# Kernel tuning notes

Hardware: AMD Instinct MI355X
Metric: run time of the kernel (lower is better)

## Reference

```python
import jax, jax.numpy as jnp
import numpy as np

H = 1024; NH = 16; HD = H // NH  # hidden, heads, head_dim

def setup_inputs() -> dict:
    key = jax.random.key(0)
    ks = jax.random.split(key, 9)
    s = 1.0 / np.sqrt(H)
    return {
        "hidden_states": jax.random.normal(ks[0], (2, 2048, H), jnp.float32),
        "Wq": jax.random.uniform(ks[1], (H, H), jnp.float32, -s, s),
        "bq": jnp.zeros((H,), jnp.float32),
        "Wk": jax.random.uniform(ks[2], (H, H), jnp.float32, -s, s),
        "bk": jnp.zeros((H,), jnp.float32),
        "Wv": jax.random.uniform(ks[3], (H, H), jnp.float32, -s, s),
        "bv": jnp.zeros((H,), jnp.float32),
        "Wo": jax.random.uniform(ks[4], (H, H), jnp.float32, -s, s),
        "bo": jnp.zeros((H,), jnp.float32),
    }

def reference(hidden_states, Wq, bq, Wk, bk, Wv, bv, Wo, bo):
    B, S, _ = hidden_states.shape
    def heads(x):  # [B,S,H] -> [B,NH,S,HD]
        return x.reshape(B, S, NH, HD).transpose(0, 2, 1, 3)
    q = heads(hidden_states @ Wq + bq)
    k = heads(hidden_states @ Wk + bk)
    v = heads(hidden_states @ Wv + bv)
    scores = jnp.einsum('bhqd,bhkd->bhqk', q, k) / jnp.sqrt(jnp.float32(HD))
    causal = jnp.where(jnp.tril(jnp.ones((S, S), bool)), 0.0, -jnp.inf)
    probs = jax.nn.softmax(scores + causal[None, None], axis=-1)
    ctx = jnp.einsum('bhqk,bhkd->bhqd', probs, v)
    ctx = ctx.transpose(0, 2, 1, 3).reshape(B, S, H)
    return ctx @ Wo + bo
```

## Files before the change

### kernel.cpp

```cpp
#include <hip/hip_runtime.h>
#include <hip/hip_bf16.h>

#define BB 2
#define SS 2048
#define HH 1024
#define NHH 16
#define HDD 64
#define MM (BB*SS)
#define QKV_N (3*HH)

typedef _Float16 f16x8 __attribute__((ext_vector_type(8)));
typedef _Float16 f16x4 __attribute__((ext_vector_type(4)));
typedef float f32x4 __attribute__((ext_vector_type(4)));

#define MFMA16(a,b,c)  __builtin_amdgcn_mfma_f32_16x16x32_f16((a),(b),(c),0,0,0)
#define MFMA16K16(a,b,c) __builtin_amdgcn_mfma_f32_16x16x16f16((a),(b),(c),0,0,0)

__device__ __forceinline__ void gl2lds16(const _Float16* g, _Float16* l) {
    __builtin_amdgcn_global_load_lds(
        (const __attribute__((address_space(1))) void*)g,
        (__attribute__((address_space(3))) void*)l, 16, 0, 0);
}

__device__ __forceinline__ float fexp2(float x) { return __builtin_amdgcn_exp2f(x); }

__global__ __launch_bounds__(256) void prep_kernel(
    const float* __restrict__ X,
    const float* __restrict__ W0, const float* __restrict__ W1,
    const float* __restrict__ W2, const float* __restrict__ W3,
    _Float16* __restrict__ Xh,
    _Float16* __restrict__ WqkvT, _Float16* __restrict__ WoT)
{
    __shared__ float t[64][65];
    int z = blockIdx.z;
    int tid = threadIdx.x;
    if (z == 4) {
        int base = (blockIdx.y * 16 + blockIdx.x) * 256 + tid;
        const float4* xin = (const float4*)X;
        f16x4* xout = (f16x4*)Xh;
#pragma unroll
        for (int i = 0; i < 16; ++i) {
            float4 v = xin[base + i * 65536];
            f16x4 hh = {(_Float16)v.x, (_Float16)v.y, (_Float16)v.z, (_Float16)v.w};
            xout[base + i * 65536] = hh;
        }
        return;
    }
    const float* src = (z == 0) ? W0 : (z == 1) ? W1 : (z == 2) ? W2 : W3;
    _Float16* dst = (z < 3) ? (WqkvT + (size_t)z * HH * HH) : WoT;
    int k0 = blockIdx.y * 64, n0 = blockIdx.x * 64;
#pragma unroll
    for (int p = 0; p < 4; ++p) {
        int row = p * 16 + (tid >> 4);
        int col4 = (tid & 15) * 4;
        float4 v = *(const float4*)&src[(size_t)(k0 + row) * HH + n0 + col4];
        t[row][col4 + 0] = v.x; t[row][col4 + 1] = v.y;
        t[row][col4 + 2] = v.z; t[row][col4 + 3] = v.w;
    }
    __syncthreads();
#pragma unroll
    for (int p = 0; p < 2; ++p) {
        int nc = p * 32 + (tid >> 3);
        int ch = tid & 7;
        f16x8 o;
#pragma unroll
        for (int j = 0; j < 8; ++j) o[j] = (_Float16)t[ch * 8 + j][nc];
        *(f16x8*)&dst[(size_t)(n0 + nc) * HH + k0 + ch * 8] = o;
    }
}

__global__ __launch_bounds__(256, 5) void gemm_qkv_kernel(
    const _Float16* __restrict__ A, const _Float16* __restrict__ Bt,
    const float* __restrict__ bias0, const float* __restrict__ bias1, const float* __restrict__ bias2,
    _Float16* __restrict__ Qh, _Float16* __restrict__ Kh, _Float16* __restrict__ Vt)
{
    const int K = HH;
    const int NT = K / 32;
    __shared__ _Float16 smem[16384];

    int row0 = blockIdx.y * 128, n0 = blockIdx.x * 128;
    int tid = threadIdx.x;
    int w = tid >> 6, l = tid & 63, m16 = l & 15, quad = l >> 4;
    int wm = w >> 1, wn = w & 1;

    int srow = w * 32 + (l >> 2);
    int sch = (l & 3) ^ ((l >> 2) & 3) ^ ((l >> 4) & 3);
    const _Float16* aptr = A + (size_t)(row0 + srow) * K + sch * 8;
    const _Float16* bptr = Bt + (size_t)(n0 + srow) * K + sch * 8;

    int gsw = (m16 & 3) ^ ((m16 >> 2) & 3);
    int acol = (quad ^ gsw) * 8;

    f32x4 zero4 = {0.f, 0.f, 0.f, 0.f};
    f32x4 acc[4][4];
#pragma unroll
    for (int i = 0; i < 4; ++i)
#pragma unroll
        for (int j = 0; j < 4; ++j) acc[i][j] = zero4;

    auto stage = [&](int t) {
        int s = (t & 1) * 4096;
        int k0 = t * 32;
        int ao = s + (w * 32) * 32;
        int bo = 8192 + s + (w * 32) * 32;
        gl2lds16(aptr + k0, smem + ao);
        gl2lds16(aptr + (size_t)16 * K + k0, smem + ao + 16 * 32);
        gl2lds16(bptr + k0, smem + bo);
        gl2lds16(bptr + (size_t)16 * K + k0, smem + bo + 16 * 32);
    };

    stage(0);
    for (int t = 0; t < NT; ++t) {
        asm volatile("s_barrier" ::: "memory");
        if (t + 1 < NT) {
            stage(t + 1);
            asm volatile("s_waitcnt vmcnt(4)" ::: "memory");
        } else {
            asm volatile("s_waitcnt vmcnt(0)" ::: "memory");
        }
        asm volatile("s_barrier" ::: "memory");

        const _Float16* Asr = smem + (t & 1) * 4096;
        const _Float16* Bsr = smem + 8192 + (t & 1) * 4096;
        f16x8 af[4], bf[4];
#pragma unroll
        for (int i = 0; i < 4; ++i)
            af[i] = *(const f16x8*)&Asr[(wm * 64 + i * 16 + m16) * 32 + acol];
#pragma unroll
        for (int j = 0; j < 4; ++j)
            bf[j] = *(const f16x8*)&Bsr[(wn * 64 + j * 16 + m16) * 32 + acol];
#pragma unroll
        for (int i = 0; i < 4; ++i)
#pragma unroll
            for (int j = 0; j < 4; ++j)
                acc[i][j] = MFMA16(af[i], bf[j], acc[i][j]);
    }

    int which = n0 >> 10;
    const float* bias = (which == 0) ? bias0 : (which == 1) ? bias1 : bias2;
    int b = row0 >> 11, s0 = row0 & 2047;

#pragma unroll
    for (int rh = 0; rh < 2; ++rh) {
        __syncthreads();
        if (wm == rh) {
#pragma unroll
            for (int j = 0; j < 4; ++j) {
                int n_local = wn * 64 + j * 16 + m16;
                float bi = bias[(n0 + n_local) & 1023];
#pragma unroll
                for (int i = 0; i < 4; ++i)
#pragma unroll
                    for (int r = 0; r < 4; ++r) {
                        int m_loc = i * 16 + quad * 4 + r;
                        float v = acc[i][j][r] + bi;
                        if (which == 0) v *= 0.18033688011112042f;
                        if (which == 2) smem[n_local * 68 + m_loc] = (_Float16)v;
                        else            smem[m_loc * 132 + n_local] = (_Float16)v;
                    }
            }
        }
        __syncthreads();
        int hs0 = s0 + rh * 64;
        if (which == 2) {
#pragma unroll
            for (int p = 0; p < 4; ++p) {
                int n_local = p * 32 + (tid >> 3);
                int schunk = tid & 7;
                f16x8 v = *(const f16x8*)&smem[n_local * 68 + schunk * 8];
                int nw = (n0 + n_local) & 1023;
                int hh = nw >> 6, d = nw & 63;
                *(f16x8*)&Vt[((size_t)(b * NHH + hh) * HDD + d) * SS + hs0 + schunk * 8] = v;
            }
        } else {
            _Float16* dst = (which == 0) ? Qh : Kh;
            int hh0 = (n0 & 1023) >> 6;
#pragma unroll
            for (int p = 0; p < 4; ++p) {
                int m_local = p * 16 + (tid >> 4);
                int seg = tid & 15;
                f16x8 v = *(const f16x8*)&smem[m_local * 132 + seg * 8];
                int hh = hh0 + (seg >> 3), d = (seg & 7) * 8;
                *(f16x8*)&dst[((size_t)(b * NHH + hh) * SS + hs0 + m_local) * HDD + d] = v;
            }
        }
    }
}

__global__ __launch_bounds__(256) void gemm_out_kernel(
    const _Float16* __restrict__ A, const _Float16* __restrict__ Bt,
    const float* __restrict__ bias0, float* __restrict__ Out)
{
    const int K = HH;
    const int NT = K / 32;
    __shared__ _Float16 smem[24576];

    int row0 = blockIdx.y * 128, n0 = blockIdx.x * 128;
    int tid = threadIdx.x;
    int w = tid >> 6, l = tid & 63, m16 = l & 15, quad = l >> 4;
    int wm = w >> 1, wn = w & 1;

    int srow = w * 32 + (l >> 2);
    int sch = (l & 3) ^ ((l >> 2) & 3) ^ ((l >> 4) & 3);
    const _Float16* aptr = A + (size_t)(row0 + srow) * K + sch * 8;
    const _Float16* bptr = Bt + (size_t)(n0 + srow) * K + sch * 8;

    int gsw = (m16 & 3) ^ ((m16 >> 2) & 3);
    int acol = (quad ^ gsw) * 8;

    f32x4 zero4 = {0.f, 0.f, 0.f, 0.f};
    f32x4 acc[4][4];
#pragma unroll
    for (int i = 0; i < 4; ++i)
#pragma unroll
        for (int j = 0; j < 4; ++j) acc[i][j] = zero4;

    auto stage = [&](int t, int s) {
        int k0 = t * 32;
        int ao = s * 4096 + (w * 32) * 32;
        int bo = 12288 + s * 4096 + (w * 32) * 32;
        gl2lds16(aptr + k0, smem + ao);
        gl2lds16(aptr + (size_t)16 * K + k0, smem + ao + 16 * 32);
        gl2lds16(bptr + k0, smem + bo);
        gl2lds16(bptr + (size_t)16 * K + k0, smem + bo + 16 * 32);
    };

    stage(0, 0);
    stage(1, 1);
    int cur = 0;
    for (int t = 0; t < NT; ++t) {
        if (t < NT - 1) asm volatile("s_waitcnt vmcnt(4)" ::: "memory");
        else            asm volatile("s_waitcnt vmcnt(0)" ::: "memory");
        asm volatile("s_barrier" ::: "memory");
        if (t + 2 < NT) {
            int nxt = cur + 2; if (nxt >= 3) nxt -= 3;
            stage(t + 2, nxt);
        }
        const _Float16* Asr = smem + cur * 4096;
        const _Float16* Bsr = smem + 12288 + cur * 4096;
        f16x8 af[4], bf[4];
#pragma unroll
        for (int i = 0; i < 4; ++i)
            af[i] = *(const f16x8*)&Asr[(wm * 64 + i * 16 + m16) * 32 + acol];
#pragma unroll
        for (int j = 0; j < 4; ++j)
            bf[j] = *(const f16x8*)&Bsr[(wn * 64 + j * 16 + m16) * 32 + acol];
#pragma unroll
        for (int i = 0; i < 4; ++i)
#pragma unroll
            for (int j = 0; j < 4; ++j)
                acc[i][j] = MFMA16(af[i], bf[j], acc[i][j]);
        cur = (cur == 2) ? 0 : cur + 1;
    }

#pragma unroll
    for (int j = 0; j < 4; ++j) {
        int n = n0 + wn * 64 + j * 16 + m16;
        float bi = bias0[n];
#pragma unroll
        for (int i = 0; i < 4; ++i)
#pragma unroll
            for (int r = 0; r < 4; ++r) {
                int mg = row0 + wm * 64 + i * 16 + quad * 4 + r;
                Out[(size_t)mg * HH + n] = acc[i][j][r] + bi;
            }
    }
}

__global__ __launch_bounds__(512, 4) void attn_kernel(
    const _Float16* __restrict__ Qh, const _Float16* __restrict__ Kh,
    const _Float16* __restrict__ Vt, _Float16* __restrict__ Ctx)
{
    __shared__ _Float16 KV[3 * 8192];

    int tid = threadIdx.x;
    int w = tid >> 6, l = tid & 63;
    int m16 = l & 15, quad = l >> 4;
    int b = blockIdx.z, h = blockIdx.y;
    int tA = blockIdx.x, tB = 31 - tA;
    int half = w >> 2, wq = w & 3;
    int myT = half ? tB : tA;

    const _Float16* Q = Qh + (size_t)(b * NHH + h) * SS * HDD;
    const _Float16* K = Kh + (size_t)(b * NHH + h) * SS * HDD;
    const _Float16* V = Vt + (size_t)(b * NHH + h) * HDD * SS;

    int q = myT * 64 + wq * 16 + m16;
    f16x8 aq0 = *(const f16x8*)(Q + (size_t)q * HDD + quad * 8);
    f16x8 aq1 = *(const f16x8*)(Q + (size_t)q * HDD + 32 + quad * 8);

    int srow = w * 8 + (l >> 3);
    int sch = (l & 7) ^ (l >> 3);
    const _Float16* kg = K + (size_t)srow * HDD + sch * 8;
    const _Float16* vg = V + (size_t)srow * SS + sch * 8;

    auto stage = [&](int t, int s) {
        int kt = t * 64;
        _Float16* kb = &KV[s * 8192];
        _Float16* vb = &KV[s * 8192 + 4096];
        gl2lds16(kg + (size_t)kt * HDD, kb + (w * 8) * 64);
        gl2lds16(vg + kt, vb + (w * 8) * 64);
    };

    int swz = m16 & 7;
    int cka = (quad ^ swz) * 8;
    int ckb = ((quad + 4) ^ swz) * 8;
    int vco[4];
#pragma unroll
    for (int s = 0; s < 4; ++s)
        vco[s] = (((s * 2 + (quad >> 1)) ^ swz) * 8) + (quad & 1) * 4;

    f32x4 zero4 = {0.f, 0.f, 0.f, 0.f};
    const f16x4 ones4 = {(_Float16)1.f, (_Float16)1.f, (_Float16)1.f, (_Float16)1.f};
    f32x4 o[4];
#pragma unroll
    for (int c = 0; c < 4; ++c) o[c] = zero4;
    f32x4 lacc = zero4;

    stage(0, 0);
    stage(1, 1);
    int cur = 0;
    for (int t = 0; t <= tB; ++t) {
        int kt = t * 64;
        if (t < tB) asm volatile("s_waitcnt vmcnt(2)" ::: "memory");
        else        asm volatile("s_waitcnt vmcnt(0)" ::: "memory");
        asm volatile("s_barrier" ::: "memory");
        if (t + 2 <= tB) {
            int nxt = cur + 2; if (nxt >= 3) nxt -= 3;
            stage(t + 2, nxt);
        }

        if (t <= myT) {
            const _Float16* kb = &KV[cur * 8192];
            const _Float16* vb = &KV[cur * 8192 + 4096];
            f16x8 bk[4][2];
#pragma unroll
            for (int s = 0; s < 4; ++s) {
                const _Float16* kr = kb + (s * 16 + m16) * 64;
                bk[s][0] = *(const f16x8*)(kr + cka);
                bk[s][1] = *(const f16x8*)(kr + ckb);
            }
            f16x4 av[4][4];
#pragma unroll
            for (int c = 0; c < 4; ++c) {
                const _Float16* vr = vb + (c * 16 + m16) * 64;
#pragma unroll
                for (int s = 0; s < 4; ++s)
                    av[c][s] = *(const f16x4*)(vr + vco[s]);
            }

            f32x4 st[4];
#pragma unroll
            for (int s = 0; s < 4; ++s) {
                st[s] = MFMA16(bk[s][0], aq0, zero4);
                st[s] = MFMA16(bk[s][1], aq1, st[s]);
            }
            f16x4 pt[4];
            if (t == myT) {
#pragma unroll
                for (int s = 0; s < 4; ++s)
#pragma unroll
                    for (int r = 0; r < 4; ++r) {
                        float p = fexp2(st[s][r]);
                        int key = kt + s * 16 + quad * 4 + r;
                        if (key > q) p = 0.f;
                        pt[s][r] = (_Float16)p;
                    }
            } else {
#pragma unroll
                for (int s = 0; s < 4; ++s)
#pragma unroll
                    for (int r = 0; r < 4; ++r)
                        pt[s][r] = (_Float16)fexp2(st[s][r]);
            }
#pragma unroll
            for (int s = 0; s < 4; ++s)
                lacc = MFMA16K16(ones4, pt[s], lacc);
#pragma unroll
            for (int c = 0; c < 4; ++c)
#pragma unroll
                for (int s = 0; s < 4; ++s)
                    o[c] = MFMA16K16(av[c][s], pt[s], o[c]);
        }

        cur = (cur == 2) ? 0 : cur + 1;
    }

    float inv = 1.0f / lacc[0];
    size_t rowoff = ((size_t)(b * SS) + q) * HH + h * HDD;
#pragma unroll
    for (int c = 0; c < 4; ++c) {
        f16x4 ov;
#pragma unroll
        for (int r = 0; r < 4; ++r) ov[r] = (_Float16)(o[c][r] * inv);
        *(f16x4*)&Ctx[rowoff + c * 16 + quad * 4] = ov;
    }
}

extern "C" void kernel_launch(void* const* d_in, const int* in_sizes, int n_in,
                              void* d_out, int out_size, void* d_ws, size_t ws_size,
                              hipStream_t stream) {
    const float* hs = (const float*)d_in[0];
    const float* Wq = (const float*)d_in[1];
    const float* bq = (const float*)d_in[2];
    const float* Wk = (const float*)d_in[3];
    const float* bk = (const float*)d_in[4];
    const float* Wv = (const float*)d_in[5];
    const float* bv = (const float*)d_in[6];
    const float* Wo = (const float*)d_in[7];
    const float* bo = (const float*)d_in[8];
    float* out = (float*)d_out;

    size_t off = 0;
    auto alloc = [&](size_t bytes) {
        void* p = (char*)d_ws + off;
        off += (bytes + 255) & ~(size_t)255;
        return p;
    };
    _Float16* Xh    = (_Float16*)alloc((size_t)MM * HH * 2);
    _Float16* WqkvT = (_Float16*)alloc((size_t)3 * HH * HH * 2);
    _Float16* WoT   = (_Float16*)alloc((size_t)HH * HH * 2);
    _Float16* Qh    = (_Float16*)alloc((size_t)BB * NHH * SS * HDD * 2);
    _Float16* Kh    = (_Float16*)alloc((size_t)BB * NHH * SS * HDD * 2);
    _Float16* Vt    = (_Float16*)alloc((size_t)BB * NHH * SS * HDD * 2);
    _Float16* Ctx   = (_Float16*)alloc((size_t)MM * HH * 2);

    prep_kernel<<<dim3(16, 16, 5), 256, 0, stream>>>(
        hs, Wq, Wk, Wv, Wo, Xh, WqkvT, WoT);
    gemm_qkv_kernel<<<dim3(QKV_N / 128, MM / 128), 256, 0, stream>>>(
        Xh, WqkvT, bq, bk, bv, Qh, Kh, Vt);
    attn_kernel<<<dim3(16, NHH, BB), 512, 0, stream>>>(Qh, Kh, Vt, Ctx);
    gemm_out_kernel<<<dim3(HH / 128, MM / 128), 256, 0, stream>>>(
        Ctx, WoT, bo, out);
}
```

Measured before the change: 181.3 us.

## Split-K output GEMM with atomics, reuse out-GEMM pipeline for QKV, pair attention tiles

The output projection GEMM is split along K into two halves, and the partial sums are accumulated into a zeroed output with atomicAdd. The zeroing is added as a new z-slice of the prep kernel. The QKV GEMM now uses the 3-stage pipelined body from the out GEMM, with a single full-tile epilogue. The attention kernel now has both wave groups process both query tiles over alternating key tiles from a shared double-buffered pair, then merges partial outputs through LDS. This aims to raise parallelism and balance work, at the cost of atomic traffic and extra LDS reductions.

```diff
diff --git a/kernel.cpp b/kernel.cpp
--- a/kernel.cpp
+++ b/kernel.cpp
@@ -29,7 +29,8 @@
     const float* __restrict__ W0, const float* __restrict__ W1,
     const float* __restrict__ W2, const float* __restrict__ W3,
     _Float16* __restrict__ Xh,
-    _Float16* __restrict__ WqkvT, _Float16* __restrict__ WoT)
+    _Float16* __restrict__ WqkvT, _Float16* __restrict__ WoT,
+    float* __restrict__ OutZ)
 {
     __shared__ float t[64][65];
     int z = blockIdx.z;
@@ -46,6 +47,14 @@
         }
         return;
     }
+    if (z == 5) {
+        int base = (blockIdx.y * 16 + blockIdx.x) * 256 + tid;
+        float4* o4 = (float4*)OutZ;
+        float4 zv = {0.f, 0.f, 0.f, 0.f};
+#pragma unroll
+        for (int i = 0; i < 16; ++i) o4[base + i * 65536] = zv;
+        return;
+    }
     const float* src = (z == 0) ? W0 : (z == 1) ? W1 : (z == 2) ? W2 : W3;
     _Float16* dst = (z < 3) ? (WqkvT + (size_t)z * HH * HH) : WoT;
     int k0 = blockIdx.y * 64, n0 = blockIdx.x * 64;
@@ -69,127 +78,10 @@
     }
 }
 
-__global__ __launch_bounds__(256, 5) void gemm_qkv_kernel(
+__global__ __launch_bounds__(256) void gemm_qkv_kernel(
     const _Float16* __restrict__ A, const _Float16* __restrict__ Bt,
     const float* __restrict__ bias0, const float* __restrict__ bias1, const float* __restrict__ bias2,
     _Float16* __restrict__ Qh, _Float16* __restrict__ Kh, _Float16* __restrict__ Vt)
-{
-    const int K = HH;
-    const int NT = K / 32;
-    __shared__ _Float16 smem[16384];
-
-    int row0 = blockIdx.y * 128, n0 = blockIdx.x * 128;
-    int tid = threadIdx.x;
-    int w = tid >> 6, l = tid & 63, m16 = l & 15, quad = l >> 4;
-    int wm = w >> 1, wn = w & 1;
-
-    int srow = w * 32 + (l >> 2);
-    int sch = (l & 3) ^ ((l >> 2) & 3) ^ ((l >> 4) & 3);
-    const _Float16* aptr = A + (size_t)(row0 + srow) * K + sch * 8;
-    const _Float16* bptr = Bt + (size_t)(n0 + srow) * K + sch * 8;
-
-    int gsw = (m16 & 3) ^ ((m16 >> 2) & 3);
-    int acol = (quad ^ gsw) * 8;
-
-    f32x4 zero4 = {0.f, 0.f, 0.f, 0.f};
-    f32x4 acc[4][4];
-#pragma unroll
-    for (int i = 0; i < 4; ++i)
-#pragma unroll
-        for (int j = 0; j < 4; ++j) acc[i][j] = zero4;
-
-    auto stage = [&](int t) {
-        int s = (t & 1) * 4096;
-        int k0 = t * 32;
-        int ao = s + (w * 32) * 32;
-        int bo = 8192 + s + (w * 32) * 32;
-        gl2lds16(aptr + k0, smem + ao);
-        gl2lds16(aptr + (size_t)16 * K + k0, smem + ao + 16 * 32);
-        gl2lds16(bptr + k0, smem + bo);
-        gl2lds16(bptr + (size_t)16 * K + k0, smem + bo + 16 * 32);
-    };
-
-    stage(0);
-    for (int t = 0; t < NT; ++t) {
-        asm volatile("s_barrier" ::: "memory");
-        if (t + 1 < NT) {
-            stage(t + 1);
-            asm volatile("s_waitcnt vmcnt(4)" ::: "memory");
-        } else {
-            asm volatile("s_waitcnt vmcnt(0)" ::: "memory");
-        }
-        asm volatile("s_barrier" ::: "memory");
-
-        const _Float16* Asr = smem + (t & 1) * 4096;
-        const _Float16* Bsr = smem + 8192 + (t & 1) * 4096;
-        f16x8 af[4], bf[4];
-#pragma unroll
-        for (int i = 0; i < 4; ++i)
-            af[i] = *(const f16x8*)&Asr[(wm * 64 + i * 16 + m16) * 32 + acol];
-#pragma unroll
-        for (int j = 0; j < 4; ++j)
-            bf[j] = *(const f16x8*)&Bsr[(wn * 64 + j * 16 + m16) * 32 + acol];
-#pragma unroll
-        for (int i = 0; i < 4; ++i)
-#pragma unroll
-            for (int j = 0; j < 4; ++j)
-                acc[i][j] = MFMA16(af[i], bf[j], acc[i][j]);
-    }
-
-    int which = n0 >> 10;
-    const float* bias = (which == 0) ? bias0 : (which == 1) ? bias1 : bias2;
-    int b = row0 >> 11, s0 = row0 & 2047;
-
-#pragma unroll
-    for (int rh = 0; rh < 2; ++rh) {
-        __syncthreads();
-        if (wm == rh) {
-#pragma unroll
-            for (int j = 0; j < 4; ++j) {
-                int n_local = wn * 64 + j * 16 + m16;
-                float bi = bias[(n0 + n_local) & 1023];
-#pragma unroll
-                for (int i = 0; i < 4; ++i)
-#pragma unroll
-                    for (int r = 0; r < 4; ++r) {
-                        int m_loc = i * 16 + quad * 4 + r;
-                        float v = acc[i][j][r] + bi;
-                        if (which == 0) v *= 0.18033688011112042f;
-                        if (which == 2) smem[n_local * 68 + m_loc] = (_Float16)v;
-                        else            smem[m_loc * 132 + n_local] = (_Float16)v;
-                    }
-            }
-        }
-        __syncthreads();
-        int hs0 = s0 + rh * 64;
-        if (which == 2) {
-#pragma unroll
-            for (int p = 0; p < 4; ++p) {
-                int n_local = p * 32 + (tid >> 3);
-                int schunk = tid & 7;
-                f16x8 v = *(const f16x8*)&smem[n_local * 68 + schunk * 8];
-                int nw = (n0 + n_local) & 1023;
-                int hh = nw >> 6, d = nw & 63;
-                *(f16x8*)&Vt[((size_t)(b * NHH + hh) * HDD + d) * SS + hs0 + schunk * 8] = v;
-            }
-        } else {
-            _Float16* dst = (which == 0) ? Qh : Kh;
-            int hh0 = (n0 & 1023) >> 6;
-#pragma unroll
-            for (int p = 0; p < 4; ++p) {
-                int m_local = p * 16 + (tid >> 4);
-                int seg = tid & 15;
-                f16x8 v = *(const f16x8*)&smem[m_local * 132 + seg * 8];
-                int hh = hh0 + (seg >> 3), d = (seg & 7) * 8;
-                *(f16x8*)&dst[((size_t)(b * NHH + hh) * SS + hs0 + m_local) * HDD + d] = v;
-            }
-        }
-    }
-}
-
-__global__ __launch_bounds__(256) void gemm_out_kernel(
-    const _Float16* __restrict__ A, const _Float16* __restrict__ Bt,
-    const float* __restrict__ bias0, float* __restrict__ Out)
 {
     const int K = HH;
     const int NT = K / 32;
@@ -253,16 +145,129 @@
         cur = (cur == 2) ? 0 : cur + 1;
     }
 
+    int which = n0 >> 10;
+    const float* bias = (which == 0) ? bias0 : (which == 1) ? bias1 : bias2;
+    __syncthreads();
+#pragma unroll
+    for (int j = 0; j < 4; ++j) {
+        int n_local = wn * 64 + j * 16 + m16;
+        float bi = bias[(n0 + n_local) & 1023];
+#pragma unroll
+        for (int i = 0; i < 4; ++i)
+#pragma unroll
+            for (int r = 0; r < 4; ++r) {
+                int m_local = wm * 64 + i * 16 + quad * 4 + r;
+                float v = acc[i][j][r] + bi;
+                if (which == 0) v *= 0.18033688011112042f;
+                if (which == 2) smem[n_local * 132 + m_local] = (_Float16)v;
+                else            smem[m_local * 132 + n_local] = (_Float16)v;
+            }
+    }
+    __syncthreads();
+
+    int b = row0 >> 11, s0 = row0 & 2047;
+    if (which == 2) {
+#pragma unroll
+        for (int p = 0; p < 8; ++p) {
+            int n_local = p * 16 + (tid >> 4);
+            int schunk = tid & 15;
+            f16x8 v = *(const f16x8*)&smem[n_local * 132 + schunk * 8];
+            int nw = (n0 + n_local) & 1023;
+            int hh = nw >> 6, d = nw & 63;
+            *(f16x8*)&Vt[((size_t)(b * NHH + hh) * HDD + d) * SS + s0 + schunk * 8] = v;
+        }
+    } else {
+        _Float16* dst = (which == 0) ? Qh : Kh;
+        int hh0 = (n0 & 1023) >> 6;
+#pragma unroll
+        for (int p = 0; p < 8; ++p) {
+            int m_local = p * 16 + (tid >> 4);
+            int seg = tid & 15;
+            f16x8 v = *(const f16x8*)&smem[m_local * 132 + seg * 8];
+            int hh = hh0 + (seg >> 3), d = (seg & 7) * 8;
+            *(f16x8*)&dst[((size_t)(b * NHH + hh) * SS + s0 + m_local) * HDD + d] = v;
+        }
+    }
+}
+
+__global__ __launch_bounds__(256) void gemm_out_kernel(
+    const _Float16* __restrict__ A, const _Float16* __restrict__ Bt,
+    const float* __restrict__ bias0, float* __restrict__ Out)
+{
+    const int K = HH;
+    const int NT = 16;
+    __shared__ _Float16 smem[24576];
+
+    int row0 = blockIdx.y * 128, n0 = blockIdx.x * 128;
+    int kbase = blockIdx.z * 512;
+    int tid = threadIdx.x;
+    int w = tid >> 6, l = tid & 63, m16 = l & 15, quad = l >> 4;
+    int wm = w >> 1, wn = w & 1;
+
+    int srow = w * 32 + (l >> 2);
+    int sch = (l & 3) ^ ((l >> 2) & 3) ^ ((l >> 4) & 3);
+    const _Float16* aptr = A + (size_t)(row0 + srow) * K + kbase + sch * 8;
+    const _Float16* bptr = Bt + (size_t)(n0 + srow) * K + kbase + sch * 8;
+
+    int gsw = (m16 & 3) ^ ((m16 >> 2) & 3);
+    int acol = (quad ^ gsw) * 8;
+
+    f32x4 zero4 = {0.f, 0.f, 0.f, 0.f};
+    f32x4 acc[4][4];
+#pragma unroll
+    for (int i = 0; i < 4; ++i)
+#pragma unroll
+        for (int j = 0; j < 4; ++j) acc[i][j] = zero4;
+
+    auto stage = [&](int t, int s) {
+        int k0 = t * 32;
+        int ao = s * 4096 + (w * 32) * 32;
+        int bo = 12288 + s * 4096 + (w * 32) * 32;
+        gl2lds16(aptr + k0, smem + ao);
+        gl2lds16(aptr + (size_t)16 * K + k0, smem + ao + 16 * 32);
+        gl2lds16(bptr + k0, smem + bo);
+        gl2lds16(bptr + (size_t)16 * K + k0, smem + bo + 16 * 32);
+    };
+
+    stage(0, 0);
+    stage(1, 1);
+    int cur = 0;
+    for (int t = 0; t < NT; ++t) {
+        if (t < NT - 1) asm volatile("s_waitcnt vmcnt(4)" ::: "memory");
+        else            asm volatile("s_waitcnt vmcnt(0)" ::: "memory");
+        asm volatile("s_barrier" ::: "memory");
+        if (t + 2 < NT) {
+            int nxt = cur + 2; if (nxt >= 3) nxt -= 3;
+            stage(t + 2, nxt);
+        }
+        const _Float16* Asr = smem + cur * 4096;
+        const _Float16* Bsr = smem + 12288 + cur * 4096;
+        f16x8 af[4], bf[4];
+#pragma unroll
+        for (int i = 0; i < 4; ++i)
+            af[i] = *(const f16x8*)&Asr[(wm * 64 + i * 16 + m16) * 32 + acol];
+#pragma unroll
+        for (int j = 0; j < 4; ++j)
+            bf[j] = *(const f16x8*)&Bsr[(wn * 64 + j * 16 + m16) * 32 + acol];
+#pragma unroll
+        for (int i = 0; i < 4; ++i)
+#pragma unroll
+            for (int j = 0; j < 4; ++j)
+                acc[i][j] = MFMA16(af[i], bf[j], acc[i][j]);
+        cur = (cur == 2) ? 0 : cur + 1;
+    }
+
+    bool addb = (blockIdx.z == 0);
 #pragma unroll
     for (int j = 0; j < 4; ++j) {
         int n = n0 + wn * 64 + j * 16 + m16;
-        float bi = bias0[n];
+        float bi = addb ? bias0[n] : 0.f;
 #pragma unroll
         for (int i = 0; i < 4; ++i)
 #pragma unroll
             for (int r = 0; r < 4; ++r) {
                 int mg = row0 + wm * 64 + i * 16 + quad * 4 + r;
-                Out[(size_t)mg * HH + n] = acc[i][j][r] + bi;
+                atomicAdd(&Out[(size_t)mg * HH + n], acc[i][j][r] + bi);
             }
     }
 }
@@ -271,35 +276,38 @@
     const _Float16* __restrict__ Qh, const _Float16* __restrict__ Kh,
     const _Float16* __restrict__ Vt, _Float16* __restrict__ Ctx)
 {
-    __shared__ _Float16 KV[3 * 8192];
+    __shared__ _Float16 KV[32768];
 
     int tid = threadIdx.x;
     int w = tid >> 6, l = tid & 63;
     int m16 = l & 15, quad = l >> 4;
     int b = blockIdx.z, h = blockIdx.y;
     int tA = blockIdx.x, tB = 31 - tA;
-    int half = w >> 2, wq = w & 3;
-    int myT = half ? tB : tA;
+    int g = w >> 2, wq = w & 3;
 
     const _Float16* Q = Qh + (size_t)(b * NHH + h) * SS * HDD;
     const _Float16* K = Kh + (size_t)(b * NHH + h) * SS * HDD;
     const _Float16* V = Vt + (size_t)(b * NHH + h) * HDD * SS;
 
-    int q = myT * 64 + wq * 16 + m16;
-    f16x8 aq0 = *(const f16x8*)(Q + (size_t)q * HDD + quad * 8);
-    f16x8 aq1 = *(const f16x8*)(Q + (size_t)q * HDD + 32 + quad * 8);
+    int qA = tA * 64 + wq * 16 + m16;
+    int qB = tB * 64 + wq * 16 + m16;
+    f16x8 aqA0 = *(const f16x8*)(Q + (size_t)qA * HDD + quad * 8);
+    f16x8 aqA1 = *(const f16x8*)(Q + (size_t)qA * HDD + 32 + quad * 8);
+    f16x8 aqB0 = *(const f16x8*)(Q + (size_t)qB * HDD + quad * 8);
+    f16x8 aqB1 = *(const f16x8*)(Q + (size_t)qB * HDD + 32 + quad * 8);
 
     int srow = w * 8 + (l >> 3);
     int sch = (l & 7) ^ (l >> 3);
     const _Float16* kg = K + (size_t)srow * HDD + sch * 8;
     const _Float16* vg = V + (size_t)srow * SS + sch * 8;
 
-    auto stage = [&](int t, int s) {
-        int kt = t * 64;
-        _Float16* kb = &KV[s * 8192];
-        _Float16* vb = &KV[s * 8192 + 4096];
-        gl2lds16(kg + (size_t)kt * HDD, kb + (w * 8) * 64);
-        gl2lds16(vg + kt, vb + (w * 8) * 64);
+    auto stage_pair = [&](int p) {
+        _Float16* base = &KV[(p & 1) * 16384];
+        int t0 = p * 128;
+        gl2lds16(kg + (size_t)t0 * HDD,        base + (w * 8) * 64);
+        gl2lds16(vg + t0,                      base + 4096 + (w * 8) * 64);
+        gl2lds16(kg + (size_t)(t0 + 64) * HDD, base + 8192 + (w * 8) * 64);
+        gl2lds16(vg + t0 + 64,                 base + 12288 + (w * 8) * 64);
     };
 
     int swz = m16 & 7;
@@ -312,27 +320,28 @@
 
     f32x4 zero4 = {0.f, 0.f, 0.f, 0.f};
     const f16x4 ones4 = {(_Float16)1.f, (_Float16)1.f, (_Float16)1.f, (_Float16)1.f};
-    f32x4 o[4];
-#pragma unroll
-    for (int c = 0; c < 4; ++c) o[c] = zero4;
-    f32x4 lacc = zero4;
-
-    stage(0, 0);
-    stage(1, 1);
-    int cur = 0;
-    for (int t = 0; t <= tB; ++t) {
-        int kt = t * 64;
-        if (t < tB) asm volatile("s_waitcnt vmcnt(2)" ::: "memory");
-        else        asm volatile("s_waitcnt vmcnt(0)" ::: "memory");
+    f32x4 oA[4], oB[4];
+#pragma unroll
+    for (int c = 0; c < 4; ++c) { oA[c] = zero4; oB[c] = zero4; }
+    f32x4 laccA = zero4, laccB = zero4;
+
+    int NIT = (tB >> 1) + 1;
+    stage_pair(0);
+    for (int it = 0; it < NIT; ++it) {
         asm volatile("s_barrier" ::: "memory");
-        if (t + 2 <= tB) {
-            int nxt = cur + 2; if (nxt >= 3) nxt -= 3;
-            stage(t + 2, nxt);
-        }
-
-        if (t <= myT) {
-            const _Float16* kb = &KV[cur * 8192];
-            const _Float16* vb = &KV[cur * 8192 + 4096];
+        if (2 * (it + 1) <= tB) {
+            stage_pair(it + 1);
+            asm volatile("s_waitcnt vmcnt(4)" ::: "memory");
+        } else {
+            asm volatile("s_waitcnt vmcnt(0)" ::: "memory");
+        }
+        asm volatile("s_barrier" ::: "memory");
+
+        int t = 2 * it + g;
+        if (t <= tB) {
+            int kt = t * 64;
+            const _Float16* kb = &KV[(it & 1) * 16384 + g * 8192];
+            const _Float16* vb = kb + 4096;
             f16x8 bk[4][2];
 #pragma unroll
             for (int s = 0; s < 4; ++s) {
@@ -349,50 +358,63 @@
                     av[c][s] = *(const f16x4*)(vr + vco[s]);
             }
 
-            f32x4 st[4];
-#pragma unroll
-            for (int s = 0; s < 4; ++s) {
-                st[s] = MFMA16(bk[s][0], aq0, zero4);
-                st[s] = MFMA16(bk[s][1], aq1, st[s]);
-            }
-            f16x4 pt[4];
-            if (t == myT) {
-#pragma unroll
-                for (int s = 0; s < 4; ++s)
+            auto body = [&](const f16x8& q0, const f16x8& q1, int qlane,
+                            f32x4* o, f32x4& lacc, bool masked) {
+                f32x4 st[4];
+#pragma unroll
+                for (int s = 0; s < 4; ++s) {
+                    st[s] = MFMA16(bk[s][0], q0, zero4);
+                    st[s] = MFMA16(bk[s][1], q1, st[s]);
+                }
+                f16x4 pt[4];
+#pragma unroll
+                for (int s = 0; s < 4; ++s) {
 #pragma unroll
                     for (int r = 0; r < 4; ++r) {
                         float p = fexp2(st[s][r]);
-                        int key = kt + s * 16 + quad * 4 + r;
-                        if (key > q) p = 0.f;
+                        if (masked) {
+                            int key = kt + s * 16 + quad * 4 + r;
+                            if (key > qlane) p = 0.f;
+                        }
                         pt[s][r] = (_Float16)p;
                     }
-            } else {
-#pragma unroll
-                for (int s = 0; s < 4; ++s)
-#pragma unroll
-                    for (int r = 0; r < 4; ++r)
-                        pt[s][r] = (_Float16)fexp2(st[s][r]);
-            }
-#pragma unroll
-            for (int s = 0; s < 4; ++s)
-                lacc = MFMA16K16(ones4, pt[s], lacc);
-#pragma unroll
-            for (int c = 0; c < 4; ++c)
-#pragma unroll
-                for (int s = 0; s < 4; ++s)
-                    o[c] = MFMA16K16(av[c][s], pt[s], o[c]);
-        }
-
-        cur = (cur == 2) ? 0 : cur + 1;
-    }
-
-    float inv = 1.0f / lacc[0];
+                    lacc = MFMA16K16(ones4, pt[s], lacc);
+                }
+#pragma unroll
+                for (int c = 0; c < 4; ++c)
+#pragma unroll
+                    for (int s = 0; s < 4; ++s)
+                        o[c] = MFMA16K16(av[c][s], pt[s], o[c]);
+            };
+
+            body(aqB0, aqB1, qB, oB, laccB, t == tB);
+            if (t <= tA) body(aqA0, aqA1, qA, oA, laccA, t == tA);
+        }
+    }
+
+    float* ox = (float*)KV;
+    float* lx = (float*)&KV[16384];
+    __syncthreads();
+    f32x4* slot = (f32x4*)(ox + ((w * 64 + l) * 16));
+#pragma unroll
+    for (int c = 0; c < 4; ++c) slot[c] = g ? oA[c] : oB[c];
+    lx[w * 64 + l] = g ? laccA[0] : laccB[0];
+    __syncthreads();
+    int pw = w ^ 4;
+    const f32x4* pslot = (const f32x4*)(ox + ((pw * 64 + l) * 16));
+    f32x4 of[4];
+#pragma unroll
+    for (int c = 0; c < 4; ++c) of[c] = (g ? oB[c] : oA[c]) + pslot[c];
+    float lf = (g ? laccB[0] : laccA[0]) + lx[pw * 64 + l];
+
+    int q = g ? qB : qA;
+    float inv = 1.0f / lf;
     size_t rowoff = ((size_t)(b * SS) + q) * HH + h * HDD;
 #pragma unroll
     for (int c = 0; c < 4; ++c) {
         f16x4 ov;
 #pragma unroll
-        for (int r = 0; r < 4; ++r) ov[r] = (_Float16)(o[c][r] * inv);
+        for (int r = 0; r < 4; ++r) ov[r] = (_Float16)(of[c][r] * inv);
         *(f16x4*)&Ctx[rowoff + c * 16 + quad * 4] = ov;
     }
 }
@@ -425,11 +447,11 @@
     _Float16* Vt    = (_Float16*)alloc((size_t)BB * NHH * SS * HDD * 2);
     _Float16* Ctx   = (_Float16*)alloc((size_t)MM * HH * 2);
 
-    prep_kernel<<<dim3(16, 16, 5), 256, 0, stream>>>(
-        hs, Wq, Wk, Wv, Wo, Xh, WqkvT, WoT);
+    prep_kernel<<<dim3(16, 16, 6), 256, 0, stream>>>(
+        hs, Wq, Wk, Wv, Wo, Xh, WqkvT, WoT, out);
     gemm_qkv_kernel<<<dim3(QKV_N / 128, MM / 128), 256, 0, stream>>>(
         Xh, WqkvT, bq, bk, bv, Qh, Kh, Vt);
     attn_kernel<<<dim3(16, NHH, BB), 512, 0, stream>>>(Qh, Kh, Vt, Ctx);
-    gemm_out_kernel<<<dim3(HH / 128, MM / 128), 256, 0, stream>>>(
+    gemm_out_kernel<<<dim3(HH / 128, MM / 128, 2), 256, 0, stream>>>(
         Ctx, WoT, bo, out);
 }
```

Result: slower. 251.0 us (+38.5%).
